# Kernel optimization log

Measured on AMD Instinct MI355X. Metric: run time of the kernel, lower is better.

## Reference

```python
import jax, jax.numpy as jnp
import numpy as np

E = 8          # num routed experts
TOP_K = 2      # experts per token
SCALE = 1.0    # routed_scaling_factor


def _swiglu(x, wg, wu, wd):
    # x: [T, D]; wg, wu: [H, D]; wd: [D, H]
    gate = jax.nn.silu(x @ wg.T)
    up = x @ wu.T
    return (gate * up) @ wd.T


def setup_inputs() -> dict:
    key = jax.random.key(0)
    ks = jax.random.split(key, 8)
    B, L, D, H = 2, 2048, 1024, 2048
    s = 0.02  # init scale for weights
    return {
        "x": jax.random.normal(ks[0], (B, L, D), jnp.float32),
        "gate_w": jax.random.normal(ks[1], (E, D), jnp.float32) * s,
        "sh_gate": jax.random.normal(ks[2], (H, D), jnp.float32) * s,
        "sh_up": jax.random.normal(ks[3], (H, D), jnp.float32) * s,
        "sh_down": jax.random.normal(ks[4], (D, H), jnp.float32) * s,
        "eg": jax.random.normal(ks[5], (E, H, D), jnp.float32) * s,
        "eu": jax.random.normal(ks[6], (E, H, D), jnp.float32) * s,
        "ed": jax.random.normal(ks[7], (E, D, H), jnp.float32) * s,
    }


def reference(x, gate_w, sh_gate, sh_up, sh_down, eg, eu, ed):
    B, L, D = x.shape
    T = B * L
    xf = x.reshape(T, D)

    # --- shared expert (num_shared_experts = 1, so the /1 average is identity) ---
    shared = _swiglu(xf, sh_gate, sh_up, sh_down)

    # --- MoE gate (inference mode: no jitter, no aux loss) ---
    router_logits = xf @ gate_w.T                                   # [T, E]
    router_probs = jax.nn.softmax(router_logits.astype(jnp.float32), axis=-1)
    w, idx = jax.lax.top_k(router_probs, TOP_K)                     # [T, K]
    w = w / jnp.sum(w, axis=-1, keepdims=True)
    w = w.astype(x.dtype)

    # per-token combine weights over experts: [T, E]
    comb = jnp.zeros((T, E), dtype=x.dtype).at[
        jnp.arange(T)[:, None], idx].add(w)

    # --- routed experts: dense stacked SwiGLU, zero-weight experts contribute 0 ---
    g = jax.nn.silu(jnp.einsum('td,ehd->teh', xf, eg))              # [T, E, H]
    u = jnp.einsum('td,ehd->teh', xf, eu)                           # [T, E, H]
    eo = jnp.einsum('teh,edh->ted', g * u, ed)                      # [T, E, D]
    routed = jnp.einsum('ted,te->td', eo, comb)                     # [T, D]

    out = shared + SCALE * routed
    return out.reshape(B, L, D)
```

## Files before the change

### kernel.cpp

```cpp
#include <hip/hip_runtime.h>

#define T_TOK 4096
#define DDIM  1024
#define HDIM  2048
#define NEXP  8
#define CAP   13312

typedef short bf16x8 __attribute__((ext_vector_type(8)));
typedef float f32x4  __attribute__((ext_vector_type(4)));

#define WS_XB   ((size_t)0)
#define WS_HBUF (WS_XB   + (size_t)T_TOK*DDIM*2)
#define WS_BTOK (WS_HBUF + (size_t)CAP*HDIM*2)
#define WS_BW   (WS_BTOK + (size_t)CAP*4)
#define WS_IDX  (WS_BW   + (size_t)CAP*4)
#define WS_WTOP (WS_IDX  + (size_t)2*T_TOK*4)
#define WS_CNT  (WS_WTOP + (size_t)2*T_TOK*4)
#define WS_OFF  (WS_CNT  + (size_t)64)
#define WS_END  (WS_OFF  + (size_t)64)

static __device__ __forceinline__ unsigned short f2bf(float f) {
  unsigned u = __float_as_uint(f);
  unsigned r = (u + 0x7FFFu + ((u >> 16) & 1u)) >> 16;
  return (unsigned short)r;
}

__global__ __launch_bounds__(256) void k_sentinel(float* __restrict__ out) {
  int gid = blockIdx.x * 256 + threadIdx.x;
  int stride = gridDim.x * 256;
  for (int i = gid; i < T_TOK * DDIM; i += stride) out[i] = 1.0e6f;
}

__global__ __launch_bounds__(256) void k_init(float* __restrict__ out,
                                              int* __restrict__ btok,
                                              int* __restrict__ cnt) {
  int gid = blockIdx.x * 256 + threadIdx.x;
  int stride = gridDim.x * 256;
  float4 z = make_float4(0.f, 0.f, 0.f, 0.f);
  for (int i = gid; i < T_TOK * DDIM / 4; i += stride) ((float4*)out)[i] = z;
  for (int i = gid; i < CAP; i += stride) btok[i] = -1;
  if (gid < 16) cnt[gid] = 0;
}

__global__ __launch_bounds__(256) void k_router(const float* __restrict__ x,
                                                const float* __restrict__ gw,
                                                unsigned short* __restrict__ xb,
                                                int* __restrict__ idx,
                                                float* __restrict__ wtop,
                                                int* __restrict__ counts) {
  int t = blockIdx.x;
  int tid = threadIdx.x;
  float4 xv = ((const float4*)(x + (size_t)t * DDIM))[tid];
  ushort4 xbv = make_ushort4(f2bf(xv.x), f2bf(xv.y), f2bf(xv.z), f2bf(xv.w));
  ((ushort4*)xb)[(size_t)t * (DDIM / 4) + tid] = xbv;

  float p[NEXP];
#pragma unroll
  for (int e = 0; e < NEXP; e++) {
    float4 g = ((const float4*)(gw + (size_t)e * DDIM))[tid];
    p[e] = xv.x * g.x + xv.y * g.y + xv.z * g.z + xv.w * g.w;
  }
#pragma unroll
  for (int e = 0; e < NEXP; e++)
    for (int off = 32; off; off >>= 1) p[e] += __shfl_down(p[e], off, 64);

  __shared__ float red[NEXP][4];
  int lane = tid & 63, wv = tid >> 6;
  if (lane == 0) {
#pragma unroll
    for (int e = 0; e < NEXP; e++) red[e][wv] = p[e];
  }
  __syncthreads();
  if (tid == 0) {
    float l[NEXP];
#pragma unroll
    for (int e = 0; e < NEXP; e++) l[e] = red[e][0] + red[e][1] + red[e][2] + red[e][3];
    int e1 = 0;
#pragma unroll
    for (int e = 1; e < NEXP; e++) if (l[e] > l[e1]) e1 = e;
    int e2 = -1;
#pragma unroll
    for (int e = 0; e < NEXP; e++) {
      if (e == e1) continue;
      if (e2 < 0 || l[e] > l[e2]) e2 = e;
    }
    float p2 = __expf(l[e2] - l[e1]);
    float s = 1.f + p2;
    idx[2 * t] = e1; idx[2 * t + 1] = e2;
    wtop[2 * t] = 1.f / s; wtop[2 * t + 1] = p2 / s;
    atomicAdd(&counts[e1], 1);
    atomicAdd(&counts[e2], 1);
  }
}

__global__ void k_offsets(const int* __restrict__ counts, int* __restrict__ off) {
  if (threadIdx.x == 0 && blockIdx.x == 0) {
    int o = 0;
    for (int e = 0; e < NEXP; e++) { off[e] = o; o += ((counts[e] + 127) >> 7) << 7; }
    off[8] = o;
    off[9] = o + T_TOK;
  }
}

__global__ __launch_bounds__(256) void k_scatter(const int* __restrict__ idx,
                                                 const float* __restrict__ wtop,
                                                 const int* __restrict__ off,
                                                 int* __restrict__ fill,
                                                 int* __restrict__ btok,
                                                 float* __restrict__ bw) {
  int t = blockIdx.x * 256 + threadIdx.x;
  if (t >= T_TOK) return;
#pragma unroll
  for (int k = 0; k < 2; k++) {
    int e = idx[2 * t + k];
    int pos = atomicAdd(&fill[e], 1);
    int d = off[e] + pos;
    btok[d] = t;
    bw[d] = wtop[2 * t + k];
  }
  int d = off[8] + t;
  btok[d] = t;
  bw[d] = 1.0f;
}

__global__ __launch_bounds__(256) void k_swiglu(const unsigned short* __restrict__ xb,
                                                const float* __restrict__ sh_gate,
                                                const float* __restrict__ sh_up,
                                                const float* __restrict__ eg,
                                                const float* __restrict__ eu,
                                                const int* __restrict__ off,
                                                const int* __restrict__ btok,
                                                unsigned short* __restrict__ hbuf) {
  __shared__ unsigned short As[128 * 72];
  __shared__ unsigned short Bg[64 * 72];
  __shared__ unsigned short Bu[64 * 72];

  int row0 = blockIdx.y * 128;
  int offv[10];
#pragma unroll
  for (int q = 0; q < 10; q++) offv[q] = off[q];
  if (row0 >= offv[9]) return;
  int e = 0;
#pragma unroll
  for (int q = 0; q < 9; q++) if (row0 >= offv[q + 1]) e = q + 1;

  const float* bgp;
  const float* bup;
  if (e < NEXP) {
    bgp = eg + (size_t)e * HDIM * DDIM;
    bup = eu + (size_t)e * HDIM * DDIM;
  } else {
    bgp = sh_gate;
    bup = sh_up;
  }
  int n0 = blockIdx.x * 64;
  int tid = threadIdx.x;

  int rtok[4];
#pragma unroll
  for (int j = 0; j < 4; j++) rtok[j] = btok[row0 + j * 32 + (tid >> 3)];

  int wid = tid >> 6, lane = tid & 63;
  int wm = wid >> 1, wn = wid & 1;
  int fr = lane & 15, fq = lane >> 4;

  f32x4 accG[4][2] = {};
  f32x4 accU[4][2] = {};

  for (int kt = 0; kt < DDIM / 64; kt++) {
#pragma unroll
    for (int j = 0; j < 4; j++) {
      int r = j * 32 + (tid >> 3), c = tid & 7;
      uint4 v = make_uint4(0, 0, 0, 0);
      if (rtok[j] >= 0)
        v = *(const uint4*)(xb + (size_t)rtok[j] * DDIM + kt * 64 + c * 8);
      *(uint4*)&As[r * 72 + c * 8] = v;
    }
#pragma unroll
    for (int j = 0; j < 4; j++) {
      int q = j * 256 + tid;
      int rb = q >> 4, c = q & 15;
      float4 vg = *(const float4*)(bgp + (size_t)(n0 + rb) * DDIM + kt * 64 + c * 4);
      float4 vu = *(const float4*)(bup + (size_t)(n0 + rb) * DDIM + kt * 64 + c * 4);
      *(ushort4*)&Bg[rb * 72 + c * 4] = make_ushort4(f2bf(vg.x), f2bf(vg.y), f2bf(vg.z), f2bf(vg.w));
      *(ushort4*)&Bu[rb * 72 + c * 4] = make_ushort4(f2bf(vu.x), f2bf(vu.y), f2bf(vu.z), f2bf(vu.w));
    }
    __syncthreads();
#pragma unroll
    for (int ks = 0; ks < 2; ks++) {
      bf16x8 a[4], bgf[2], buf_[2];
#pragma unroll
      for (int i = 0; i < 4; i++)
        a[i] = *(const bf16x8*)&As[(wm * 64 + i * 16 + fr) * 72 + ks * 32 + fq * 8];
#pragma unroll
      for (int j = 0; j < 2; j++) {
        bgf[j]  = *(const bf16x8*)&Bg[(wn * 32 + j * 16 + fr) * 72 + ks * 32 + fq * 8];
        buf_[j] = *(const bf16x8*)&Bu[(wn * 32 + j * 16 + fr) * 72 + ks * 32 + fq * 8];
      }
#pragma unroll
      for (int i = 0; i < 4; i++)
#pragma unroll
        for (int j = 0; j < 2; j++) {
          accG[i][j] = __builtin_amdgcn_mfma_f32_16x16x32_bf16(a[i], bgf[j], accG[i][j], 0, 0, 0);
          accU[i][j] = __builtin_amdgcn_mfma_f32_16x16x32_bf16(a[i], buf_[j], accU[i][j], 0, 0, 0);
        }
    }
    __syncthreads();
  }

#pragma unroll
  for (int i = 0; i < 4; i++)
#pragma unroll
    for (int j = 0; j < 2; j++)
#pragma unroll
      for (int r = 0; r < 4; r++) {
        float g = accG[i][j][r], u = accU[i][j][r];
        float h = g / (1.f + __expf(-g)) * u;
        int row = row0 + wm * 64 + i * 16 + fq * 4 + r;
        int col = n0 + wn * 32 + j * 16 + fr;
        hbuf[(size_t)row * HDIM + col] = f2bf(h);
      }
}

__global__ __launch_bounds__(256) void k_down(const unsigned short* __restrict__ hbuf,
                                              const float* __restrict__ sh_down,
                                              const float* __restrict__ ed,
                                              const int* __restrict__ off,
                                              const int* __restrict__ btok,
                                              const float* __restrict__ bw,
                                              float* __restrict__ out) {
  __shared__ unsigned short As[128 * 72];
  __shared__ unsigned short Bs[128 * 72];

  int row0 = blockIdx.y * 128;
  int offv[10];
#pragma unroll
  for (int q = 0; q < 10; q++) offv[q] = off[q];
  if (row0 >= offv[9]) return;
  int e = 0;
#pragma unroll
  for (int q = 0; q < 9; q++) if (row0 >= offv[q + 1]) e = q + 1;

  const float* bd = (e < NEXP) ? (ed + (size_t)e * DDIM * HDIM) : sh_down;
  int n0 = blockIdx.x * 128;
  int tid = threadIdx.x;
  int wid = tid >> 6, lane = tid & 63;
  int wm = wid >> 1, wn = wid & 1;
  int fr = lane & 15, fq = lane >> 4;

  f32x4 acc[4][4] = {};

  for (int kt = 0; kt < HDIM / 64; kt++) {
#pragma unroll
    for (int j = 0; j < 4; j++) {
      int r = j * 32 + (tid >> 3), c = tid & 7;
      *(uint4*)&As[r * 72 + c * 8] =
          *(const uint4*)(hbuf + (size_t)(row0 + r) * HDIM + kt * 64 + c * 8);
    }
#pragma unroll
    for (int j = 0; j < 8; j++) {
      int q = j * 256 + tid;
      int rb = q >> 4, c = q & 15;
      float4 v = *(const float4*)(bd + (size_t)(n0 + rb) * HDIM + kt * 64 + c * 4);
      *(ushort4*)&Bs[rb * 72 + c * 4] = make_ushort4(f2bf(v.x), f2bf(v.y), f2bf(v.z), f2bf(v.w));
    }
    __syncthreads();
#pragma unroll
    for (int ks = 0; ks < 2; ks++) {
      bf16x8 a[4], b[4];
#pragma unroll
      for (int i = 0; i < 4; i++)
        a[i] = *(const bf16x8*)&As[(wm * 64 + i * 16 + fr) * 72 + ks * 32 + fq * 8];
#pragma unroll
      for (int j = 0; j < 4; j++)
        b[j] = *(const bf16x8*)&Bs[(wn * 64 + j * 16 + fr) * 72 + ks * 32 + fq * 8];
#pragma unroll
      for (int i = 0; i < 4; i++)
#pragma unroll
        for (int j = 0; j < 4; j++)
          acc[i][j] = __builtin_amdgcn_mfma_f32_16x16x32_bf16(a[i], b[j], acc[i][j], 0, 0, 0);
    }
    __syncthreads();
  }

#pragma unroll
  for (int i = 0; i < 4; i++)
#pragma unroll
    for (int r = 0; r < 4; r++) {
      int brow = row0 + wm * 64 + i * 16 + fq * 4 + r;
      int tok = btok[brow];
      if (tok < 0) continue;
      float w = bw[brow];
#pragma unroll
      for (int j = 0; j < 4; j++) {
        int col = n0 + wn * 64 + j * 16 + fr;
        atomicAdd(&out[(size_t)tok * DDIM + col], w * acc[i][j][r]);
      }
    }
}

extern "C" void kernel_launch(void* const* d_in, const int* in_sizes, int n_in,
                              void* d_out, int out_size, void* d_ws, size_t ws_size,
                              hipStream_t stream) {
  const float* x       = (const float*)d_in[0];
  const float* gw      = (const float*)d_in[1];
  const float* sh_gate = (const float*)d_in[2];
  const float* sh_up   = (const float*)d_in[3];
  const float* sh_down = (const float*)d_in[4];
  const float* eg      = (const float*)d_in[5];
  const float* eu      = (const float*)d_in[6];
  const float* ed      = (const float*)d_in[7];
  float* out = (float*)d_out;
  char* ws = (char*)d_ws;

  if (ws_size < WS_END) {
    hipLaunchKernelGGL(k_sentinel, dim3(1024), dim3(256), 0, stream, out);
    return;
  }

  unsigned short* xb   = (unsigned short*)(ws + WS_XB);
  unsigned short* hbuf = (unsigned short*)(ws + WS_HBUF);
  int*   btok  = (int*)(ws + WS_BTOK);
  float* bw    = (float*)(ws + WS_BW);
  int*   idx   = (int*)(ws + WS_IDX);
  float* wtop  = (float*)(ws + WS_WTOP);
  int*   cnt   = (int*)(ws + WS_CNT);
  int*   fill  = cnt + 8;
  int*   off   = (int*)(ws + WS_OFF);

  hipLaunchKernelGGL(k_init,    dim3(2048), dim3(256), 0, stream, out, btok, cnt);
  hipLaunchKernelGGL(k_router,  dim3(T_TOK), dim3(256), 0, stream, x, gw, xb, idx, wtop, cnt);
  hipLaunchKernelGGL(k_offsets, dim3(1), dim3(64), 0, stream, cnt, off);
  hipLaunchKernelGGL(k_scatter, dim3(T_TOK / 256), dim3(256), 0, stream, idx, wtop, off, fill, btok, bw);
  hipLaunchKernelGGL(k_swiglu,  dim3(HDIM / 64, CAP / 128), dim3(256), 0, stream,
                     xb, sh_gate, sh_up, eg, eu, off, btok, hbuf);
  hipLaunchKernelGGL(k_down,    dim3(DDIM / 128, CAP / 128), dim3(256), 0, stream,
                     hbuf, sh_down, ed, off, btok, bw, out);
}
```

Measured before the change: 769.3 us.

## Pre-convert weights to bf16 and load tiles via global_load_lds with swizzled LDS

```diff
diff --git a/kernel.cpp b/kernel.cpp
--- a/kernel.cpp
+++ b/kernel.cpp
@@ -19,12 +19,36 @@
 #define WS_OFF  (WS_CNT  + (size_t)64)
 #define WS_END  (WS_OFF  + (size_t)64)
 
+#define NEW_EXP ((size_t)NEXP*HDIM*DDIM)
+#define NSH     ((size_t)HDIM*DDIM)
+#define WS2_XB   ((size_t)0)
+#define WS2_HBUF (WS2_XB   + (size_t)T_TOK*DDIM*2)
+#define WS2_EGB  (WS2_HBUF + (size_t)CAP*HDIM*2)
+#define WS2_EUB  (WS2_EGB  + NEW_EXP*2)
+#define WS2_EDB  (WS2_EUB  + NEW_EXP*2)
+#define WS2_SGB  (WS2_EDB  + NEW_EXP*2)
+#define WS2_SUB  (WS2_SGB  + NSH*2)
+#define WS2_SDB  (WS2_SUB  + NSH*2)
+#define WS2_BTOK (WS2_SDB  + NSH*2)
+#define WS2_BW   (WS2_BTOK + (size_t)CAP*4)
+#define WS2_IDX  (WS2_BW   + (size_t)CAP*4)
+#define WS2_WTOP (WS2_IDX  + (size_t)2*T_TOK*4)
+#define WS2_CNT  (WS2_WTOP + (size_t)2*T_TOK*4)
+#define WS2_OFF  (WS2_CNT  + (size_t)64)
+#define WS2_ZROW (WS2_OFF  + (size_t)64)
+#define WS2_END  (WS2_ZROW + (size_t)4096)
+
 static __device__ __forceinline__ unsigned short f2bf(float f) {
   unsigned u = __float_as_uint(f);
   unsigned r = (u + 0x7FFFu + ((u >> 16) & 1u)) >> 16;
   return (unsigned short)r;
 }
 
+static __device__ __forceinline__ void gll16(const void* g, void* l) {
+  __builtin_amdgcn_global_load_lds((const __attribute__((address_space(1))) void*)g,
+                                   (__attribute__((address_space(3))) void*)l, 16, 0, 0);
+}
+
 __global__ __launch_bounds__(256) void k_sentinel(float* __restrict__ out) {
   int gid = blockIdx.x * 256 + threadIdx.x;
   int stride = gridDim.x * 256;
@@ -33,13 +57,46 @@
 
 __global__ __launch_bounds__(256) void k_init(float* __restrict__ out,
                                               int* __restrict__ btok,
-                                              int* __restrict__ cnt) {
+                                              int* __restrict__ cnt,
+                                              unsigned int* __restrict__ zz) {
   int gid = blockIdx.x * 256 + threadIdx.x;
   int stride = gridDim.x * 256;
   float4 z = make_float4(0.f, 0.f, 0.f, 0.f);
   for (int i = gid; i < T_TOK * DDIM / 4; i += stride) ((float4*)out)[i] = z;
   for (int i = gid; i < CAP; i += stride) btok[i] = -1;
+  for (int i = gid; i < 1024; i += stride) zz[i] = 0u;
   if (gid < 16) cnt[gid] = 0;
+}
+
+#define NE8 ((long)(NEW_EXP / 8))
+#define NS8 ((long)(NSH / 8))
+__global__ __launch_bounds__(256) void k_convert(
+    const float* __restrict__ eg, const float* __restrict__ eu, const float* __restrict__ ed,
+    const float* __restrict__ sg, const float* __restrict__ su, const float* __restrict__ sd,
+    unsigned short* __restrict__ egb, unsigned short* __restrict__ eub, unsigned short* __restrict__ edb,
+    unsigned short* __restrict__ sgb, unsigned short* __restrict__ sub, unsigned short* __restrict__ sdb) {
+  long gid = (long)blockIdx.x * 256 + threadIdx.x;
+  long stride = (long)gridDim.x * 256;
+  const long TOT8 = 3 * NE8 + 3 * NS8;
+  for (long i = gid; i < TOT8; i += stride) {
+    const float* s; unsigned short* d; long o;
+    if (i < 3 * NE8) {
+      long a = i >> 21, r = i & (NE8 - 1);
+      s = (a == 0) ? eg : ((a == 1) ? eu : ed);
+      d = (a == 0) ? egb : ((a == 1) ? eub : edb);
+      o = r;
+    } else {
+      long b = i - 3 * NE8;
+      long a = b >> 18, r = b & (NS8 - 1);
+      s = (a == 0) ? sg : ((a == 1) ? su : sd);
+      d = (a == 0) ? sgb : ((a == 1) ? sub : sdb);
+      o = r;
+    }
+    float4 v0 = ((const float4*)s)[o * 2];
+    float4 v1 = ((const float4*)s)[o * 2 + 1];
+    ((ushort4*)d)[o * 2]     = make_ushort4(f2bf(v0.x), f2bf(v0.y), f2bf(v0.z), f2bf(v0.w));
+    ((ushort4*)d)[o * 2 + 1] = make_ushort4(f2bf(v1.x), f2bf(v1.y), f2bf(v1.z), f2bf(v1.w));
+  }
 }
 
 __global__ __launch_bounds__(256) void k_router(const float* __restrict__ x,
@@ -123,6 +180,191 @@
   bw[d] = 1.0f;
 }
 
+
+__global__ __launch_bounds__(256) void k_swiglu2(const unsigned short* __restrict__ xb,
+                                                 const unsigned short* __restrict__ sgb,
+                                                 const unsigned short* __restrict__ sub,
+                                                 const unsigned short* __restrict__ egb,
+                                                 const unsigned short* __restrict__ eub,
+                                                 const int* __restrict__ off,
+                                                 const int* __restrict__ btok,
+                                                 const unsigned short* __restrict__ zrow,
+                                                 unsigned short* __restrict__ hbuf) {
+  __shared__ __align__(16) unsigned short As[128 * 64];
+  __shared__ __align__(16) unsigned short Bg[64 * 64];
+  __shared__ __align__(16) unsigned short Bu[64 * 64];
+
+  int row0 = blockIdx.y * 128;
+  int offv[10];
+#pragma unroll
+  for (int q = 0; q < 10; q++) offv[q] = off[q];
+  if (row0 >= offv[9]) return;
+  int e = 0;
+#pragma unroll
+  for (int q = 0; q < 9; q++) if (row0 >= offv[q + 1]) e = q + 1;
+
+  const unsigned short* bgp = (e < NEXP) ? (egb + (size_t)e * HDIM * DDIM) : sgb;
+  const unsigned short* bup = (e < NEXP) ? (eub + (size_t)e * HDIM * DDIM) : sub;
+  int n0 = blockIdx.x * 64;
+  int tid = threadIdx.x;
+  int w = tid >> 6, l = tid & 63;
+  int lr = l >> 3;
+  int c  = (l & 7) ^ lr;
+
+  const unsigned short* asrc[4];
+#pragma unroll
+  for (int j = 0; j < 4; j++) {
+    int tok = btok[row0 + w * 32 + j * 8 + lr];
+    asrc[j] = ((tok >= 0) ? (xb + (size_t)tok * DDIM) : zrow) + c * 8;
+  }
+  const unsigned short* bgsrc[2];
+  const unsigned short* busrc[2];
+#pragma unroll
+  for (int j = 0; j < 2; j++) {
+    int rb = w * 16 + j * 8 + lr;
+    bgsrc[j] = bgp + (size_t)(n0 + rb) * DDIM + c * 8;
+    busrc[j] = bup + (size_t)(n0 + rb) * DDIM + c * 8;
+  }
+
+  int wm = w >> 1, wn = w & 1;
+  int fr = l & 15, fq = l >> 4;
+  int f7 = fr & 7;
+
+  f32x4 accG[4][2] = {};
+  f32x4 accU[4][2] = {};
+
+  for (int kt = 0; kt < DDIM / 64; kt++) {
+    int ko = kt * 64;
+#pragma unroll
+    for (int j = 0; j < 4; j++)
+      gll16(asrc[j] + ko, As + (w * 32 + j * 8) * 64);
+#pragma unroll
+    for (int j = 0; j < 2; j++) {
+      gll16(bgsrc[j] + ko, Bg + (w * 16 + j * 8) * 64);
+      gll16(busrc[j] + ko, Bu + (w * 16 + j * 8) * 64);
+    }
+    __syncthreads();
+#pragma unroll
+    for (int ks = 0; ks < 2; ks++) {
+      int ck = ks * 4 + fq;
+      bf16x8 a[4], bgf[2], buf_[2];
+#pragma unroll
+      for (int i = 0; i < 4; i++)
+        a[i] = *(const bf16x8*)&As[(wm * 64 + i * 16 + fr) * 64 + ((ck ^ f7) * 8)];
+#pragma unroll
+      for (int j = 0; j < 2; j++) {
+        bgf[j]  = *(const bf16x8*)&Bg[(wn * 32 + j * 16 + fr) * 64 + ((ck ^ f7) * 8)];
+        buf_[j] = *(const bf16x8*)&Bu[(wn * 32 + j * 16 + fr) * 64 + ((ck ^ f7) * 8)];
+      }
+#pragma unroll
+      for (int i = 0; i < 4; i++)
+#pragma unroll
+        for (int j = 0; j < 2; j++) {
+          accG[i][j] = __builtin_amdgcn_mfma_f32_16x16x32_bf16(a[i], bgf[j], accG[i][j], 0, 0, 0);
+          accU[i][j] = __builtin_amdgcn_mfma_f32_16x16x32_bf16(a[i], buf_[j], accU[i][j], 0, 0, 0);
+        }
+    }
+    __syncthreads();
+  }
+
+#pragma unroll
+  for (int i = 0; i < 4; i++)
+#pragma unroll
+    for (int j = 0; j < 2; j++)
+#pragma unroll
+      for (int r = 0; r < 4; r++) {
+        float g = accG[i][j][r], u = accU[i][j][r];
+        float h = g / (1.f + __expf(-g)) * u;
+        int row = row0 + wm * 64 + i * 16 + fq * 4 + r;
+        int col = n0 + wn * 32 + j * 16 + fr;
+        hbuf[(size_t)row * HDIM + col] = f2bf(h);
+      }
+}
+
+__global__ __launch_bounds__(256) void k_down2(const unsigned short* __restrict__ hbuf,
+                                               const unsigned short* __restrict__ sdb,
+                                               const unsigned short* __restrict__ edb,
+                                               const int* __restrict__ off,
+                                               const int* __restrict__ btok,
+                                               const float* __restrict__ bw,
+                                               float* __restrict__ out) {
+  __shared__ __align__(16) unsigned short As[128 * 64];
+  __shared__ __align__(16) unsigned short Bs[128 * 64];
+
+  int row0 = blockIdx.y * 128;
+  int offv[10];
+#pragma unroll
+  for (int q = 0; q < 10; q++) offv[q] = off[q];
+  if (row0 >= offv[9]) return;
+  int e = 0;
+#pragma unroll
+  for (int q = 0; q < 9; q++) if (row0 >= offv[q + 1]) e = q + 1;
+
+  const unsigned short* bd = (e < NEXP) ? (edb + (size_t)e * DDIM * HDIM) : sdb;
+  int n0 = blockIdx.x * 128;
+  int tid = threadIdx.x;
+  int w = tid >> 6, l = tid & 63;
+  int lr = l >> 3;
+  int c  = (l & 7) ^ lr;
+
+  const unsigned short* asrc[4];
+  const unsigned short* bsrc[4];
+#pragma unroll
+  for (int j = 0; j < 4; j++) {
+    int r = (w * 4 + j) * 8 + lr;
+    asrc[j] = hbuf + (size_t)(row0 + r) * HDIM + c * 8;
+    bsrc[j] = bd   + (size_t)(n0 + r) * HDIM + c * 8;
+  }
+
+  int wm = w >> 1, wn = w & 1;
+  int fr = l & 15, fq = l >> 4;
+  int f7 = fr & 7;
+
+  f32x4 acc[4][4] = {};
+
+  for (int kt = 0; kt < HDIM / 64; kt++) {
+    int ko = kt * 64;
+#pragma unroll
+    for (int j = 0; j < 4; j++) {
+      gll16(asrc[j] + ko, As + (w * 4 + j) * 8 * 64);
+      gll16(bsrc[j] + ko, Bs + (w * 4 + j) * 8 * 64);
+    }
+    __syncthreads();
+#pragma unroll
+    for (int ks = 0; ks < 2; ks++) {
+      int ck = ks * 4 + fq;
+      bf16x8 a[4], b[4];
+#pragma unroll
+      for (int i = 0; i < 4; i++)
+        a[i] = *(const bf16x8*)&As[(wm * 64 + i * 16 + fr) * 64 + ((ck ^ f7) * 8)];
+#pragma unroll
+      for (int j = 0; j < 4; j++)
+        b[j] = *(const bf16x8*)&Bs[(wn * 64 + j * 16 + fr) * 64 + ((ck ^ f7) * 8)];
+#pragma unroll
+      for (int i = 0; i < 4; i++)
+#pragma unroll
+        for (int j = 0; j < 4; j++)
+          acc[i][j] = __builtin_amdgcn_mfma_f32_16x16x32_bf16(a[i], b[j], acc[i][j], 0, 0, 0);
+    }
+    __syncthreads();
+  }
+
+#pragma unroll
+  for (int i = 0; i < 4; i++)
+#pragma unroll
+    for (int r = 0; r < 4; r++) {
+      int brow = row0 + wm * 64 + i * 16 + fq * 4 + r;
+      int tok = btok[brow];
+      if (tok < 0) continue;
+      float wgt = bw[brow];
+#pragma unroll
+      for (int j = 0; j < 4; j++) {
+        int col = n0 + wn * 64 + j * 16 + fr;
+        atomicAdd(&out[(size_t)tok * DDIM + col], wgt * acc[i][j][r]);
+      }
+    }
+}
+
 __global__ __launch_bounds__(256) void k_swiglu(const unsigned short* __restrict__ xb,
                                                 const float* __restrict__ sh_gate,
                                                 const float* __restrict__ sh_up,
@@ -170,20 +412,20 @@
   for (int kt = 0; kt < DDIM / 64; kt++) {
 #pragma unroll
     for (int j = 0; j < 4; j++) {
-      int r = j * 32 + (tid >> 3), c = tid & 7;
+      int r = j * 32 + (tid >> 3), cc = tid & 7;
       uint4 v = make_uint4(0, 0, 0, 0);
       if (rtok[j] >= 0)
-        v = *(const uint4*)(xb + (size_t)rtok[j] * DDIM + kt * 64 + c * 8);
-      *(uint4*)&As[r * 72 + c * 8] = v;
+        v = *(const uint4*)(xb + (size_t)rtok[j] * DDIM + kt * 64 + cc * 8);
+      *(uint4*)&As[r * 72 + cc * 8] = v;
     }
 #pragma unroll
     for (int j = 0; j < 4; j++) {
       int q = j * 256 + tid;
-      int rb = q >> 4, c = q & 15;
-      float4 vg = *(const float4*)(bgp + (size_t)(n0 + rb) * DDIM + kt * 64 + c * 4);
-      float4 vu = *(const float4*)(bup + (size_t)(n0 + rb) * DDIM + kt * 64 + c * 4);
-      *(ushort4*)&Bg[rb * 72 + c * 4] = make_ushort4(f2bf(vg.x), f2bf(vg.y), f2bf(vg.z), f2bf(vg.w));
-      *(ushort4*)&Bu[rb * 72 + c * 4] = make_ushort4(f2bf(vu.x), f2bf(vu.y), f2bf(vu.z), f2bf(vu.w));
+      int rb = q >> 4, cc = q & 15;
+      float4 vg = *(const float4*)(bgp + (size_t)(n0 + rb) * DDIM + kt * 64 + cc * 4);
+      float4 vu = *(const float4*)(bup + (size_t)(n0 + rb) * DDIM + kt * 64 + cc * 4);
+      *(ushort4*)&Bg[rb * 72 + cc * 4] = make_ushort4(f2bf(vg.x), f2bf(vg.y), f2bf(vg.z), f2bf(vg.w));
+      *(ushort4*)&Bu[rb * 72 + cc * 4] = make_ushort4(f2bf(vu.x), f2bf(vu.y), f2bf(vu.z), f2bf(vu.w));
     }
     __syncthreads();
 #pragma unroll
@@ -253,16 +495,16 @@
   for (int kt = 0; kt < HDIM / 64; kt++) {
 #pragma unroll
     for (int j = 0; j < 4; j++) {
-      int r = j * 32 + (tid >> 3), c = tid & 7;
-      *(uint4*)&As[r * 72 + c * 8] =
-          *(const uint4*)(hbuf + (size_t)(row0 + r) * HDIM + kt * 64 + c * 8);
+      int r = j * 32 + (tid >> 3), cc = tid & 7;
+      *(uint4*)&As[r * 72 + cc * 8] =
+          *(const uint4*)(hbuf + (size_t)(row0 + r) * HDIM + kt * 64 + cc * 8);
     }
 #pragma unroll
     for (int j = 0; j < 8; j++) {
       int q = j * 256 + tid;
-      int rb = q >> 4, c = q & 15;
-      float4 v = *(const float4*)(bd + (size_t)(n0 + rb) * HDIM + kt * 64 + c * 4);
-      *(ushort4*)&Bs[rb * 72 + c * 4] = make_ushort4(f2bf(v.x), f2bf(v.y), f2bf(v.z), f2bf(v.w));
+      int rb = q >> 4, cc = q & 15;
+      float4 v = *(const float4*)(bd + (size_t)(n0 + rb) * HDIM + kt * 64 + cc * 4);
+      *(ushort4*)&Bs[rb * 72 + cc * 4] = make_ushort4(f2bf(v.x), f2bf(v.y), f2bf(v.z), f2bf(v.w));
     }
     __syncthreads();
 #pragma unroll
@@ -313,27 +555,54 @@
   float* out = (float*)d_out;
   char* ws = (char*)d_ws;
 
-  if (ws_size < WS_END) {
+  if (ws_size >= WS2_END) {
+    unsigned short* xb   = (unsigned short*)(ws + WS2_XB);
+    unsigned short* hbuf = (unsigned short*)(ws + WS2_HBUF);
+    unsigned short* egb  = (unsigned short*)(ws + WS2_EGB);
+    unsigned short* eub  = (unsigned short*)(ws + WS2_EUB);
+    unsigned short* edb  = (unsigned short*)(ws + WS2_EDB);
+    unsigned short* sgb  = (unsigned short*)(ws + WS2_SGB);
+    unsigned short* sub  = (unsigned short*)(ws + WS2_SUB);
+    unsigned short* sdb  = (unsigned short*)(ws + WS2_SDB);
+    int*   btok  = (int*)(ws + WS2_BTOK);
+    float* bw    = (float*)(ws + WS2_BW);
+    int*   idx   = (int*)(ws + WS2_IDX);
+    float* wtop  = (float*)(ws + WS2_WTOP);
+    int*   cnt   = (int*)(ws + WS2_CNT);
+    int*   fill  = cnt + 8;
+    int*   off   = (int*)(ws + WS2_OFF);
+    unsigned short* zrow = (unsigned short*)(ws + WS2_ZROW);
+
+    hipLaunchKernelGGL(k_init,    dim3(2048), dim3(256), 0, stream, out, btok, cnt, (unsigned int*)zrow);
+    hipLaunchKernelGGL(k_convert, dim3(2048), dim3(256), 0, stream,
+                       eg, eu, ed, sh_gate, sh_up, sh_down, egb, eub, edb, sgb, sub, sdb);
+    hipLaunchKernelGGL(k_router,  dim3(T_TOK), dim3(256), 0, stream, x, gw, xb, idx, wtop, cnt);
+    hipLaunchKernelGGL(k_offsets, dim3(1), dim3(64), 0, stream, cnt, off);
+    hipLaunchKernelGGL(k_scatter, dim3(T_TOK / 256), dim3(256), 0, stream, idx, wtop, off, fill, btok, bw);
+    hipLaunchKernelGGL(k_swiglu2, dim3(HDIM / 64, CAP / 128), dim3(256), 0, stream,
+                       xb, sgb, sub, egb, eub, off, btok, zrow, hbuf);
+    hipLaunchKernelGGL(k_down2,   dim3(DDIM / 128, CAP / 128), dim3(256), 0, stream,
+                       hbuf, sdb, edb, off, btok, bw, out);
+  } else if (ws_size >= WS_END) {
+    unsigned short* xb   = (unsigned short*)(ws + WS_XB);
+    unsigned short* hbuf = (unsigned short*)(ws + WS_HBUF);
+    int*   btok  = (int*)(ws + WS_BTOK);
+    float* bw    = (float*)(ws + WS_BW);
+    int*   idx   = (int*)(ws + WS_IDX);
+    float* wtop  = (float*)(ws + WS_WTOP);
+    int*   cnt   = (int*)(ws + WS_CNT);
+    int*   fill  = cnt + 8;
+    int*   off   = (int*)(ws + WS_OFF);
+
+    hipLaunchKernelGGL(k_init,    dim3(2048), dim3(256), 0, stream, out, btok, cnt, (unsigned int*)xb);
+    hipLaunchKernelGGL(k_router,  dim3(T_TOK), dim3(256), 0, stream, x, gw, xb, idx, wtop, cnt);
+    hipLaunchKernelGGL(k_offsets, dim3(1), dim3(64), 0, stream, cnt, off);
+    hipLaunchKernelGGL(k_scatter, dim3(T_TOK / 256), dim3(256), 0, stream, idx, wtop, off, fill, btok, bw);
+    hipLaunchKernelGGL(k_swiglu,  dim3(HDIM / 64, CAP / 128), dim3(256), 0, stream,
+                       xb, sh_gate, sh_up, eg, eu, off, btok, hbuf);
+    hipLaunchKernelGGL(k_down,    dim3(DDIM / 128, CAP / 128), dim3(256), 0, stream,
+                       hbuf, sh_down, ed, off, btok, bw, out);
+  } else {
     hipLaunchKernelGGL(k_sentinel, dim3(1024), dim3(256), 0, stream, out);
-    return;
-  }
-
-  unsigned short* xb   = (unsigned short*)(ws + WS_XB);
-  unsigned short* hbuf = (unsigned short*)(ws + WS_HBUF);
-  int*   btok  = (int*)(ws + WS_BTOK);
-  float* bw    = (float*)(ws + WS_BW);
-  int*   idx   = (int*)(ws + WS_IDX);
-  float* wtop  = (float*)(ws + WS_WTOP);
-  int*   cnt   = (int*)(ws + WS_CNT);
-  int*   fill  = cnt + 8;
-  int*   off   = (int*)(ws + WS_OFF);
-
-  hipLaunchKernelGGL(k_init,    dim3(2048), dim3(256), 0, stream, out, btok, cnt);
-  hipLaunchKernelGGL(k_router,  dim3(T_TOK), dim3(256), 0, stream, x, gw, xb, idx, wtop, cnt);
-  hipLaunchKernelGGL(k_offsets, dim3(1), dim3(64), 0, stream, cnt, off);
-  hipLaunchKernelGGL(k_scatter, dim3(T_TOK / 256), dim3(256), 0, stream, idx, wtop, off, fill, btok, bw);
-  hipLaunchKernelGGL(k_swiglu,  dim3(HDIM / 64, CAP / 128), dim3(256), 0, stream,
-                     xb, sh_gate, sh_up, eg, eu, off, btok, hbuf);
-  hipLaunchKernelGGL(k_down,    dim3(DDIM / 128, CAP / 128), dim3(256), 0, stream,
-                     hbuf, sh_down, ed, off, btok, bw, out);
-}
+  }
+}
```

Result: faster. 680.5 us (-11.5%).
